# Kernel optimization log

Hardware: AMD Instinct MI355X
Metric: run time of the kernel (lower is better)

The kernel has to match this reference:

```python
import jax, jax.numpy as jnp
import numpy as np

B, C, N = 4, 256, 4096
BN_EPS = 1e-5


def setup_inputs() -> dict:
    key = jax.random.key(0)
    ks = jax.random.split(key, 8)
    Cq = C // 4
    return {
        "x": jax.random.normal(ks[0], (B, C, N), dtype=jnp.float32),
        # q_conv and k_conv share weights (self.q_conv.weight = self.k_conv.weight)
        "w_qk": jax.random.normal(ks[1], (Cq, C), dtype=jnp.float32) * 0.05,
        "w_v": jax.random.normal(ks[2], (C, C), dtype=jnp.float32) * 0.05,
        "b_v": jax.random.normal(ks[3], (C,), dtype=jnp.float32) * 0.05,
        # LBR: Conv1d(C,C,1) + BN1d (inference stats) + ReLU
        "w_lbr": jax.random.normal(ks[4], (C, C), dtype=jnp.float32) * 0.05,
        "b_lbr": jax.random.normal(ks[5], (C,), dtype=jnp.float32) * 0.05,
        "bn_gamma": jnp.ones((C,), dtype=jnp.float32),
        "bn_beta": jnp.zeros((C,), dtype=jnp.float32),
        "bn_mean": jax.random.normal(ks[6], (C,), dtype=jnp.float32) * 0.05,
        "bn_var": jax.random.uniform(ks[7], (C,), dtype=jnp.float32, minval=0.5, maxval=1.5),
    }


def reference(x, w_qk, w_v, b_v, w_lbr, b_lbr, bn_gamma, bn_beta, bn_mean, bn_var):
    # x: [B, C, N]
    chans = x.shape[1]
    # conv1x1 Q/K (shared weight, no bias), V (with bias)
    x_q = jnp.einsum('qc,bcn->bnq', w_qk, x)          # [B, N, C/4]
    x_k = jnp.einsum('qc,bcm->bqm', w_qk, x)          # [B, C/4, N]
    x_v = jnp.einsum('oc,bcn->bon', w_v, x) + b_v[None, :, None]  # [B, C, N]
    # energy: [B, N_query, N_key]
    energy = jnp.einsum('bnq,bqm->bnm', x_q, x_k)
    # 'SL' normalization: scale by C**-0.5, softmax over dim=-2 (query axis)
    energy = energy * (chans ** -0.5)
    attention = jax.nn.softmax(energy, axis=-2)        # [B, N, N]
    # x_r[b,c,m] = sum_n x_v[b,c,n] * attention[b,n,m]
    x_r = jnp.einsum('bcn,bnm->bcm', x_v, attention)   # [B, C, N]
    # offset residual
    x_r = x - x_r
    # LBR: conv1x1 -> BN (inference) -> ReLU
    h = jnp.einsum('oc,bcn->bon', w_lbr, x_r) + b_lbr[None, :, None]
    inv_std = jax.lax.rsqrt(bn_var + BN_EPS)
    h = (h - bn_mean[None, :, None]) * (inv_std * bn_gamma)[None, :, None] + bn_beta[None, :, None]
    h = jax.nn.relu(h)
    return x + h
```

## Files before the change

kernel.cpp:

```cpp
#include <hip/hip_runtime.h>
#include <hip/hip_bf16.h>
#include <stdint.h>
#include <math.h>

#define Bq 4
#define Cc 256
#define Nn 4096
#define CQ 64
#define QKSCALE 0.30028060219661246f
#define NT 64
#define NIT (Nn / NT)
#define QBUF 8704

typedef short s16x4 __attribute__((ext_vector_type(4)));
typedef short s16x8 __attribute__((ext_vector_type(8)));
typedef unsigned int u32x4 __attribute__((ext_vector_type(4)));
typedef float f32x16 __attribute__((ext_vector_type(16)));

#define MFMA32(a,b,c) __builtin_amdgcn_mfma_f32_32x32x16_bf16((a),(b),(c),0,0,0)

#define BAR_LGKM() asm volatile("s_waitcnt lgkmcnt(0)\n\ts_barrier" ::: "memory")

static __device__ __forceinline__ unsigned short f2b(float f) {
  unsigned int u = __float_as_uint(f);
  u += 0x7FFFu + ((u >> 16) & 1u);
  return (unsigned short)(u >> 16);
}

static __device__ __forceinline__ unsigned short f2bh(float f) {
  __hip_bfloat16 h = __float2bfloat16(f);
  return __builtin_bit_cast(unsigned short, h);
}

static __device__ __forceinline__ float b2f(unsigned short u) {
  return __uint_as_float(((unsigned int)u) << 16);
}

static __device__ __forceinline__ float fexp2(float x) {
#if __has_builtin(__builtin_amdgcn_exp2f)
  return __builtin_amdgcn_exp2f(x);
#else
  return exp2f(x);
#endif
}

static __device__ __forceinline__ f32x16 fz16() {
  f32x16 z;
#pragma unroll
  for (int i = 0; i < 16; i++) z[i] = 0.0f;
  return z;
}

__global__ __launch_bounds__(256) void k_prep(
    const float* __restrict__ wqk, const float* __restrict__ wv,
    const float* __restrict__ wlbr, const float* __restrict__ blbr,
    const float* __restrict__ gamma, const float* __restrict__ beta,
    const float* __restrict__ mean, const float* __restrict__ var,
    unsigned short* __restrict__ Wcat, float* __restrict__ sd,
    unsigned int* __restrict__ mxb) {
  int bx = blockIdx.x, t = threadIdx.x;
  if (bx < 576) {
    float v;
    if (bx < 64) v = wqk[bx * 256 + t] * QKSCALE;
    else if (bx < 320) v = wv[(bx - 64) * 256 + t];
    else v = wlbr[(bx - 320) * 256 + t];
    Wcat[bx * 256 + t] = f2b(v);
  } else {
    float s = gamma[t] * rsqrtf(var[t] + 1e-5f);
    sd[t] = s;
    sd[256 + t] = beta[t] + (blbr[t] - mean[t]) * s;
    if (t < 4) mxb[t] = 0u;
  }
}

__global__ __launch_bounds__(640) void k_proj(const float* __restrict__ x,
                                              const unsigned short* __restrict__ Wcat,
                                              const float* __restrict__ bv,
                                              unsigned short* __restrict__ qkT,
                                              unsigned short* __restrict__ Vf,
                                              unsigned short* __restrict__ xT) {
  __shared__ unsigned short xs[32 * 264];
  int bx = blockIdx.x;
  int b = bx >> 7;
  int ntile = bx & 127;
  int n0 = ntile * 32;
  int t = threadIdx.x;
  const float* xb = x + (size_t)b * Cc * Nn;
  for (int u = t; u < 1024; u += 640) {
    int c = u >> 2, j = (u & 3) * 8;
    const float* src = &xb[(size_t)c * Nn + n0 + j];
    float4 v0 = *(const float4*)src;
    float4 v1 = *(const float4*)(src + 4);
    xs[(j + 0) * 264 + c] = f2b(v0.x);
    xs[(j + 1) * 264 + c] = f2b(v0.y);
    xs[(j + 2) * 264 + c] = f2b(v0.z);
    xs[(j + 3) * 264 + c] = f2b(v0.w);
    xs[(j + 4) * 264 + c] = f2b(v1.x);
    xs[(j + 5) * 264 + c] = f2b(v1.y);
    xs[(j + 6) * 264 + c] = f2b(v1.z);
    xs[(j + 7) * 264 + c] = f2b(v1.w);
  }
  int w = t >> 6, a = t & 31, g = (t >> 5) & 1;
  bool isqk = (w >= 8);
  int row0 = isqk ? (w - 8) * 32 : 64 + w * 32;
  s16x8 wf[16];
#pragma unroll
  for (int kc = 0; kc < 16; kc++)
    wf[kc] = *(const s16x8*)&Wcat[(size_t)(row0 + a) * 256 + kc * 16 + 8 * g];
  __syncthreads();
  unsigned short* xTb = xT + ((size_t)b * Nn + n0) * Cc;
  for (int u = t; u < 1024; u += 640) {
    int row = u >> 5, ch = u & 31;
    *(s16x8*)&xTb[(size_t)row * Cc + ch * 8] = *(const s16x8*)&xs[row * 264 + ch * 8];
  }
  f32x16 acc = fz16();
#pragma unroll
  for (int kc = 0; kc < 16; kc++) {
    s16x8 xf = *(const s16x8*)&xs[a * 264 + kc * 16 + 8 * g];
    acc = MFMA32(xf, wf[kc], acc);
  }
  if (isqk) {
    unsigned short* dst = qkT + ((size_t)b * Nn + n0) * CQ;
    int q0 = row0;
#pragma unroll
    for (int r = 0; r < 16; r++) {
      int n = (r & 3) + 8 * (r >> 2) + 4 * g;
      dst[(size_t)n * CQ + q0 + a] = f2b(acc[r]);
    }
  } else {
    int c0 = row0 - 64;
    float bvv = bv[c0 + a];
    s16x8 vlo, vhi;
#pragma unroll
    for (int r = 0; r < 8; r++) {
      vlo[r] = (short)f2b(acc[r] + bvv);
      vhi[r] = (short)f2b(acc[8 + r] + bvv);
    }
    unsigned short* dstF =
        Vf + ((size_t)(b * 128 + ntile) * 4 + g) * 2048 + (size_t)(c0 + a) * 8;
    *(s16x8*)dstF = vlo;
    *(s16x8*)(dstF + 4096) = vhi;
  }
}

__global__ __launch_bounds__(256) void k_norm(const unsigned short* __restrict__ qkT,
                                              float* __restrict__ nrm,
                                              unsigned int* __restrict__ mxb) {
  int idx = blockIdx.x * 256 + threadIdx.x;
  const unsigned short* row = qkT + (size_t)idx * CQ;
  float s = 0.0f;
#pragma unroll
  for (int k = 0; k < 8; k++) {
    s16x8 v = *(const s16x8*)&row[k * 8];
#pragma unroll
    for (int j = 0; j < 8; j++) {
      float f = b2f((unsigned short)v[j]);
      s += f * f;
    }
  }
  float nr = sqrtf(s);
  nrm[idx] = nr;
  float m = nr;
#pragma unroll
  for (int off = 1; off < 64; off <<= 1) m = fmaxf(m, __shfl_xor(m, off, 64));
  __shared__ float wm[4];
  if ((threadIdx.x & 63) == 0) wm[threadIdx.x >> 6] = m;
  __syncthreads();
  if (threadIdx.x == 0) {
    float mm = fmaxf(fmaxf(wm[0], wm[1]), fmaxf(wm[2], wm[3]));
    atomicMax(mxb + (idx >> 12), __float_as_uint(mm));
  }
}

__global__ __launch_bounds__(512, 2) void k_attn(const unsigned short* __restrict__ qkT,
                                                 const unsigned short* __restrict__ Vf,
                                                 const float* __restrict__ nrm,
                                                 const unsigned int* __restrict__ mxb,
                                                 unsigned short* __restrict__ xT) {
  __shared__ __align__(16) char smem[33280];
  int bx = blockIdx.x;
  int id = ((bx & 7) << 6) | (bx >> 3);
  int b = id >> 7;
  int m0 = (id & 127) * 32;
  int t = threadIdx.x;
  int w = t >> 6, a = t & 31, g = (t >> 5) & 1;
  int nh = w >> 2, cs = w & 3;
  bool isProd = (w == 0) | (w == 7);
  unsigned int* Plds = (unsigned int*)(smem + 2 * QBUF);
  const unsigned short* qkTb = qkT + (size_t)b * Nn * CQ;
  int mcol = m0 + a;
  s16x8 Bqk[4];
#pragma unroll
  for (int kc = 0; kc < 4; kc++)
    Bqk[kc] = *(const s16x8*)&qkTb[(size_t)mcol * CQ + kc * 16 + 8 * g];
  float Mh = nrm[(size_t)b * Nn + mcol] * __uint_as_float(mxb[b]) + 0.01f;
  int ccol = cs * 64 + a;
  const unsigned short* Vfb = Vf + (size_t)b * 1048576 + (size_t)g * 2048;

  int qc = t & 7, qr = t >> 3;
  s16x8 qf;
#define STAGE_LOAD(nn)                                                         \
  do {                                                                         \
    qf = *(const s16x8*)&qkTb[(size_t)((nn) + qr) * CQ + qc * 8];              \
  } while (0)
#define STAGE_WRITE(bc)                                                        \
  do {                                                                         \
    unsigned short* Q_ = (unsigned short*)(smem + (bc) * QBUF);                \
    unsigned short* dq = &Q_[qr * 68 + qc * 8];                                \
    *(s16x4*)dq = __builtin_shufflevector(qf, qf, 0, 1, 2, 3);                 \
    *(s16x4*)(dq + 4) = __builtin_shufflevector(qf, qf, 4, 5, 6, 7);           \
  } while (0)

  STAGE_LOAD(0);
  STAGE_WRITE(0);
  STAGE_LOAD(NT);
  f32x16 acc0 = fz16(), acc1 = fz16();
  float Lp = 0.0f;
  BAR_LGKM();
#pragma unroll 1
  for (int ns = 0; ns < NIT; ns++) {
    int cur = ns & 1;
    const unsigned short* Vt = Vfb + (size_t)(ns * 2 + nh) * 8192;
    s16x8 vf0[2], vf1[2];
#pragma unroll
    for (int kk = 0; kk < 2; kk++) {
      vf0[kk] = *(const s16x8*)&Vt[(size_t)kk * 4096 + (size_t)ccol * 8];
      vf1[kk] = *(const s16x8*)&Vt[(size_t)kk * 4096 + (size_t)(ccol + 32) * 8];
    }
    const unsigned short* Qc = (const unsigned short*)(smem + cur * QBUF);
    s16x8 pw0, pw1;
    if (isProd) {
      f32x16 E = fz16();
#pragma unroll
      for (int kc = 0; kc < 4; kc++) {
        const unsigned short* p = &Qc[(nh * 32 + a) * 68 + kc * 16 + 8 * g];
        s16x4 lo = *(const s16x4*)p, hi = *(const s16x4*)(p + 4);
        E = MFMA32(__builtin_shufflevector(lo, hi, 0, 1, 2, 3, 4, 5, 6, 7), Bqk[kc], E);
      }
#pragma unroll
      for (int r = 0; r < 16; r++) E[r] = fexp2(E[r] - Mh);
      Lp += (((E[0] + E[1]) + (E[2] + E[3])) + ((E[4] + E[5]) + (E[6] + E[7]))) +
            (((E[8] + E[9]) + (E[10] + E[11])) + ((E[12] + E[13]) + (E[14] + E[15])));
#pragma unroll
      for (int j = 0; j < 8; j++) {
        pw0[j] = (short)f2bh(E[j]);
        pw1[j] = (short)f2bh(E[8 + j]);
      }
      u32x4 u0 = __builtin_bit_cast(u32x4, pw0);
      u32x4 u1 = __builtin_bit_cast(u32x4, pw1);
      unsigned int* Pq = Plds + nh * 512 + (t & 63);
      Pq[0] = u0[0]; Pq[64] = u0[1]; Pq[128] = u0[2]; Pq[192] = u0[3];
      Pq[256] = u1[0]; Pq[320] = u1[1]; Pq[384] = u1[2]; Pq[448] = u1[3];
    }
    if (ns + 1 < NIT) STAGE_WRITE(cur ^ 1);
    if (ns + 2 < NIT) STAGE_LOAD((ns + 2) * NT);
    BAR_LGKM();
    if (!isProd) {
      const unsigned int* Pq = Plds + nh * 512 + (t & 63);
      u32x4 u0, u1;
      u0[0] = Pq[0]; u0[1] = Pq[64]; u0[2] = Pq[128]; u0[3] = Pq[192];
      u1[0] = Pq[256]; u1[1] = Pq[320]; u1[2] = Pq[384]; u1[3] = Pq[448];
      pw0 = __builtin_bit_cast(s16x8, u0);
      pw1 = __builtin_bit_cast(s16x8, u1);
    }
#pragma unroll
    for (int kk = 0; kk < 2; kk++) {
      s16x8 pk = (kk == 0) ? pw0 : pw1;
      acc0 = MFMA32(pk, vf0[kk], acc0);
      acc1 = MFMA32(pk, vf1[kk], acc1);
    }
    BAR_LGKM();
  }
#undef STAGE_LOAD
#undef STAGE_WRITE
  float Lw = Lp + __shfl_xor(Lp, 32, 64);
  float* Pf = (float*)smem;
  float* Ls = (float*)(smem + 32768);
  if (isProd && (t & 63) < 32) Ls[nh * 32 + a] = Lw;
  if (nh == 1) {
    int base0 = cs * 2048;
#pragma unroll
    for (int r = 0; r < 16; r++) {
      int row = (r & 3) + 8 * (r >> 2) + 4 * g;
      Pf[base0 + row * 64 + a] = acc0[r];
      Pf[base0 + row * 64 + 32 + a] = acc1[r];
    }
  }
  __syncthreads();
  if (nh == 0) {
    unsigned short* xTb = xT + ((size_t)b * Nn + m0) * Cc;
    int base0 = cs * 2048;
#pragma unroll
    for (int r = 0; r < 16; r++) {
      int row = (r & 3) + 8 * (r >> 2) + 4 * g;
      float a0 = acc0[r] + Pf[base0 + row * 64 + a];
      float a1 = acc1[r] + Pf[base0 + row * 64 + 32 + a];
      float rL = 1.0f / (Ls[row] + Ls[32 + row]);
      unsigned short* p0 = &xTb[(size_t)row * Cc + cs * 64 + a];
      unsigned short* p1 = p0 + 32;
      *p0 = f2b(b2f(*p0) - a0 * rL);
      *p1 = f2b(b2f(*p1) - a1 * rL);
    }
  }
}

__global__ __launch_bounds__(512) void k_lbr(const unsigned short* __restrict__ xrT,
                                             const unsigned short* __restrict__ Wcat,
                                             const float* __restrict__ sd,
                                             const float* __restrict__ x,
                                             float* __restrict__ out) {
  __shared__ unsigned short xs[32 * 264];
  __shared__ float sL[256], dL[256];
  int bx = blockIdx.x;
  int b = bx >> 7;
  int n0 = (bx & 127) * 32;
  int t = threadIdx.x;
  const unsigned short* src = xrT + ((size_t)b * Nn + n0) * Cc;
  for (int u = t; u < 1024; u += 512) {
    int row = u >> 5, ch = u & 31;
    *(s16x8*)&xs[row * 264 + ch * 8] = *(const s16x8*)&src[row * Cc + ch * 8];
  }
  if (t < 256) {
    sL[t] = sd[t];
    dL[t] = sd[256 + t];
  }
  int w = t >> 6, a = t & 31, g = (t >> 5) & 1;
  int o0 = w * 32;
  s16x8 wf[16];
#pragma unroll
  for (int kc = 0; kc < 16; kc++)
    wf[kc] = *(const s16x8*)&Wcat[(size_t)(320 + o0 + a) * 256 + kc * 16 + 8 * g];
  __syncthreads();
  f32x16 acc = fz16();
#pragma unroll
  for (int kc = 0; kc < 16; kc++) {
    s16x8 xf = *(const s16x8*)&xs[a * 264 + kc * 16 + 8 * g];
    acc = MFMA32(wf[kc], xf, acc);
  }
  const float* xb = x + (size_t)b * Cc * Nn;
  float* ob = out + (size_t)b * Cc * Nn;
#pragma unroll
  for (int r = 0; r < 16; r++) {
    int o = o0 + (r & 3) + 8 * (r >> 2) + 4 * g;
    float v = acc[r] * sL[o] + dL[o];
    v = fmaxf(v, 0.0f);
    ob[(size_t)o * Nn + n0 + a] = xb[(size_t)o * Nn + n0 + a] + v;
  }
}

extern "C" void kernel_launch(void* const* d_in, const int* in_sizes, int n_in,
                              void* d_out, int out_size, void* d_ws, size_t ws_size,
                              hipStream_t stream) {
  (void)in_sizes; (void)n_in; (void)out_size; (void)ws_size;
  const float* x = (const float*)d_in[0];
  const float* wqk = (const float*)d_in[1];
  const float* wv = (const float*)d_in[2];
  const float* bv = (const float*)d_in[3];
  const float* wlbr = (const float*)d_in[4];
  const float* blbr = (const float*)d_in[5];
  const float* gamma = (const float*)d_in[6];
  const float* beta = (const float*)d_in[7];
  const float* mean = (const float*)d_in[8];
  const float* var = (const float*)d_in[9];
  char* ws = (char*)d_ws;
  unsigned short* qkT = (unsigned short*)ws;
  unsigned short* Vf = (unsigned short*)(ws + 2097152);
  unsigned short* xT = (unsigned short*)(ws + 10485760);
  float* sd = (float*)(ws + 18874368);
  unsigned short* Wcat = (unsigned short*)(ws + 18876416);
  float* out = (float*)d_out;
  float* nrm = (float*)d_out;
  unsigned int* mxb = (unsigned int*)((char*)d_out + 131072);

  k_prep<<<dim3(577), dim3(256), 0, stream>>>(wqk, wv, wlbr, blbr, gamma, beta,
                                              mean, var, Wcat, sd, mxb);
  k_proj<<<dim3(512), dim3(640), 0, stream>>>(x, Wcat, bv, qkT, Vf, xT);
  k_norm<<<dim3(64), dim3(256), 0, stream>>>(qkT, nrm, mxb);
  k_attn<<<dim3(512), dim3(512), 0, stream>>>(qkT, Vf, nrm, mxb, xT );
  k_lbr<<<dim3(512), dim3(512), 0, stream>>>(xT , Wcat, sd, x, out);
}
```

Before: 108.6 us.

## Restructure attention kernel: 64-column tiles, split-N waves, barrier-free main loop

```diff
diff --git a/kernel.cpp b/kernel.cpp
--- a/kernel.cpp
+++ b/kernel.cpp
@@ -8,9 +8,6 @@
 #define Nn 4096
 #define CQ 64
 #define QKSCALE 0.30028060219661246f
-#define NT 64
-#define NIT (Nn / NT)
-#define QBUF 8704
 
 typedef short s16x4 __attribute__((ext_vector_type(4)));
 typedef short s16x8 __attribute__((ext_vector_type(8)));
@@ -18,8 +15,6 @@
 typedef float f32x16 __attribute__((ext_vector_type(16)));
 
 #define MFMA32(a,b,c) __builtin_amdgcn_mfma_f32_32x32x16_bf16((a),(b),(c),0,0,0)
-
-#define BAR_LGKM() asm volatile("s_waitcnt lgkmcnt(0)\n\ts_barrier" ::: "memory")
 
 static __device__ __forceinline__ unsigned short f2b(float f) {
   unsigned int u = __float_as_uint(f);
@@ -49,6 +44,11 @@
 #pragma unroll
   for (int i = 0; i < 16; i++) z[i] = 0.0f;
   return z;
+}
+
+static __device__ __forceinline__ float sum16(f32x16 E) {
+  return (((E[0] + E[1]) + (E[2] + E[3])) + ((E[4] + E[5]) + (E[6] + E[7]))) +
+         (((E[8] + E[9]) + (E[10] + E[11])) + ((E[12] + E[13]) + (E[14] + E[15])));
 }
 
 __global__ __launch_bounds__(256) void k_prep(
@@ -177,130 +177,129 @@
                                                  const float* __restrict__ nrm,
                                                  const unsigned int* __restrict__ mxb,
                                                  unsigned short* __restrict__ xT) {
-  __shared__ __align__(16) char smem[33280];
+  __shared__ __align__(16) float Pf[4 * 128 * 33];
+  __shared__ float Ls[4 * 64];
   int bx = blockIdx.x;
-  int id = ((bx & 7) << 6) | (bx >> 3);
-  int b = id >> 7;
-  int m0 = (id & 127) * 32;
+  int id = ((bx & 7) << 5) | (bx >> 3);
+  int b = id >> 6;
+  int m0 = (id & 63) * 64;
   int t = threadIdx.x;
   int w = t >> 6, a = t & 31, g = (t >> 5) & 1;
-  int nh = w >> 2, cs = w & 3;
-  bool isProd = (w == 0) | (w == 7);
-  unsigned int* Plds = (unsigned int*)(smem + 2 * QBUF);
+  int cs = w >> 2, ns = w & 3;
   const unsigned short* qkTb = qkT + (size_t)b * Nn * CQ;
-  int mcol = m0 + a;
-  s16x8 Bqk[4];
+  s16x8 Bq0[4], Bq1[4];
+#pragma unroll
+  for (int kc = 0; kc < 4; kc++) {
+    Bq0[kc] = *(const s16x8*)&qkTb[(size_t)(m0 + a) * CQ + kc * 16 + 8 * g];
+    Bq1[kc] = *(const s16x8*)&qkTb[(size_t)(m0 + 32 + a) * CQ + kc * 16 + 8 * g];
+  }
+  float mxf = __uint_as_float(mxb[b]);
+  float Mh0 = nrm[(size_t)b * Nn + m0 + a] * mxf + 0.01f;
+  float Mh1 = nrm[(size_t)b * Nn + m0 + 32 + a] * mxf + 0.01f;
+  const unsigned short* Vc = Vf + (size_t)b * 1048576 + (size_t)g * 2048 +
+                             (size_t)(cs * 128 + a) * 8;
+  f32x16 acc[8];
+#pragma unroll
+  for (int i = 0; i < 8; i++) acc[i] = fz16();
+  float Lp0 = 0.0f, Lp1 = 0.0f;
+  s16x8 qf[4];
 #pragma unroll
   for (int kc = 0; kc < 4; kc++)
-    Bqk[kc] = *(const s16x8*)&qkTb[(size_t)mcol * CQ + kc * 16 + 8 * g];
-  float Mh = nrm[(size_t)b * Nn + mcol] * __uint_as_float(mxb[b]) + 0.01f;
-  int ccol = cs * 64 + a;
-  const unsigned short* Vfb = Vf + (size_t)b * 1048576 + (size_t)g * 2048;
-
-  int qc = t & 7, qr = t >> 3;
-  s16x8 qf;
-#define STAGE_LOAD(nn)                                                         \
-  do {                                                                         \
-    qf = *(const s16x8*)&qkTb[(size_t)((nn) + qr) * CQ + qc * 8];              \
-  } while (0)
-#define STAGE_WRITE(bc)                                                        \
-  do {                                                                         \
-    unsigned short* Q_ = (unsigned short*)(smem + (bc) * QBUF);                \
-    unsigned short* dq = &Q_[qr * 68 + qc * 8];                                \
-    *(s16x4*)dq = __builtin_shufflevector(qf, qf, 0, 1, 2, 3);                 \
-    *(s16x4*)(dq + 4) = __builtin_shufflevector(qf, qf, 4, 5, 6, 7);           \
-  } while (0)
-
-  STAGE_LOAD(0);
-  STAGE_WRITE(0);
-  STAGE_LOAD(NT);
-  f32x16 acc0 = fz16(), acc1 = fz16();
-  float Lp = 0.0f;
-  BAR_LGKM();
+    qf[kc] = *(const s16x8*)&qkTb[(size_t)(ns * 32 + a) * CQ + kc * 16 + 8 * g];
 #pragma unroll 1
-  for (int ns = 0; ns < NIT; ns++) {
-    int cur = ns & 1;
-    const unsigned short* Vt = Vfb + (size_t)(ns * 2 + nh) * 8192;
-    s16x8 vf0[2], vf1[2];
-#pragma unroll
-    for (int kk = 0; kk < 2; kk++) {
-      vf0[kk] = *(const s16x8*)&Vt[(size_t)kk * 4096 + (size_t)ccol * 8];
-      vf1[kk] = *(const s16x8*)&Vt[(size_t)kk * 4096 + (size_t)(ccol + 32) * 8];
-    }
-    const unsigned short* Qc = (const unsigned short*)(smem + cur * QBUF);
-    s16x8 pw0, pw1;
-    if (isProd) {
-      f32x16 E = fz16();
-#pragma unroll
-      for (int kc = 0; kc < 4; kc++) {
-        const unsigned short* p = &Qc[(nh * 32 + a) * 68 + kc * 16 + 8 * g];
-        s16x4 lo = *(const s16x4*)p, hi = *(const s16x4*)(p + 4);
-        E = MFMA32(__builtin_shufflevector(lo, hi, 0, 1, 2, 3, 4, 5, 6, 7), Bqk[kc], E);
+  for (int nt = ns; nt < 128; nt += 4) {
+    const unsigned short* Vt = Vc + (size_t)nt * 8192;
+    f32x16 E0 = fz16(), E1 = fz16();
+#pragma unroll
+    for (int kc = 0; kc < 4; kc++) E0 = MFMA32(qf[kc], Bq0[kc], E0);
+    s16x8 va0, va1, va2, va3;
+    va0 = *(const s16x8*)&Vt[0];
+    va1 = *(const s16x8*)&Vt[4096];
+    va2 = *(const s16x8*)&Vt[256];
+    va3 = *(const s16x8*)&Vt[4096 + 256];
+#pragma unroll
+    for (int kc = 0; kc < 4; kc++) E1 = MFMA32(qf[kc], Bq1[kc], E1);
+    int ntn = (nt + 4) & 127;
+#pragma unroll
+    for (int kc = 0; kc < 4; kc++)
+      qf[kc] = *(const s16x8*)&qkTb[(size_t)(ntn * 32 + a) * CQ + kc * 16 + 8 * g];
+#pragma unroll
+    for (int r = 0; r < 16; r++) E0[r] = fexp2(E0[r] - Mh0);
+    Lp0 += sum16(E0);
+    s16x8 p00, p01;
+#pragma unroll
+    for (int j = 0; j < 8; j++) {
+      p00[j] = (short)f2bh(E0[j]);
+      p01[j] = (short)f2bh(E0[8 + j]);
+    }
+#pragma unroll
+    for (int r = 0; r < 16; r++) E1[r] = fexp2(E1[r] - Mh1);
+    Lp1 += sum16(E1);
+    s16x8 p10, p11;
+#pragma unroll
+    for (int j = 0; j < 8; j++) {
+      p10[j] = (short)f2bh(E1[j]);
+      p11[j] = (short)f2bh(E1[8 + j]);
+    }
+    acc[0] = MFMA32(p00, va0, acc[0]);
+    acc[4] = MFMA32(p10, va0, acc[4]);
+    acc[1] = MFMA32(p00, va2, acc[1]);
+    acc[5] = MFMA32(p10, va2, acc[5]);
+    acc[0] = MFMA32(p01, va1, acc[0]);
+    acc[4] = MFMA32(p11, va1, acc[4]);
+    acc[1] = MFMA32(p01, va3, acc[1]);
+    acc[5] = MFMA32(p11, va3, acc[5]);
+    s16x8 vb0, vb1, vb2, vb3;
+    vb0 = *(const s16x8*)&Vt[512];
+    vb1 = *(const s16x8*)&Vt[4096 + 512];
+    vb2 = *(const s16x8*)&Vt[768];
+    vb3 = *(const s16x8*)&Vt[4096 + 768];
+    acc[2] = MFMA32(p00, vb0, acc[2]);
+    acc[6] = MFMA32(p10, vb0, acc[6]);
+    acc[3] = MFMA32(p00, vb2, acc[3]);
+    acc[7] = MFMA32(p10, vb2, acc[7]);
+    acc[2] = MFMA32(p01, vb1, acc[2]);
+    acc[6] = MFMA32(p11, vb1, acc[6]);
+    acc[3] = MFMA32(p01, vb3, acc[3]);
+    acc[7] = MFMA32(p11, vb3, acc[7]);
+  }
+  float Lw0 = Lp0 + __shfl_xor(Lp0, 32, 64);
+  float Lw1 = Lp1 + __shfl_xor(Lp1, 32, 64);
+  if (cs == 0 && (t & 63) < 32) {
+    Ls[ns * 64 + a] = Lw0;
+    Ls[ns * 64 + 32 + a] = Lw1;
+  }
+  unsigned short* xTb = xT + ((size_t)b * Nn + m0) * Cc;
+#pragma unroll
+  for (int q = 0; q < 4; q++) {
+    int qmt = q >> 1, qcs = q & 1;
+    __syncthreads();
+    if (cs == qcs) {
+#pragma unroll
+      for (int ct = 0; ct < 4; ct++) {
+        float* dst = &Pf[(size_t)(ns * 128 + ct * 32 + a) * 33];
+        f32x16 A = acc[qmt * 4 + ct];
+#pragma unroll
+        for (int r = 0; r < 16; r++) {
+          int mrow = (r & 3) + 8 * (r >> 2) + 4 * g;
+          dst[mrow] = A[r];
+        }
       }
-#pragma unroll
-      for (int r = 0; r < 16; r++) E[r] = fexp2(E[r] - Mh);
-      Lp += (((E[0] + E[1]) + (E[2] + E[3])) + ((E[4] + E[5]) + (E[6] + E[7]))) +
-            (((E[8] + E[9]) + (E[10] + E[11])) + ((E[12] + E[13]) + (E[14] + E[15])));
-#pragma unroll
-      for (int j = 0; j < 8; j++) {
-        pw0[j] = (short)f2bh(E[j]);
-        pw1[j] = (short)f2bh(E[8 + j]);
-      }
-      u32x4 u0 = __builtin_bit_cast(u32x4, pw0);
-      u32x4 u1 = __builtin_bit_cast(u32x4, pw1);
-      unsigned int* Pq = Plds + nh * 512 + (t & 63);
-      Pq[0] = u0[0]; Pq[64] = u0[1]; Pq[128] = u0[2]; Pq[192] = u0[3];
-      Pq[256] = u1[0]; Pq[320] = u1[1]; Pq[384] = u1[2]; Pq[448] = u1[3];
-    }
-    if (ns + 1 < NIT) STAGE_WRITE(cur ^ 1);
-    if (ns + 2 < NIT) STAGE_LOAD((ns + 2) * NT);
-    BAR_LGKM();
-    if (!isProd) {
-      const unsigned int* Pq = Plds + nh * 512 + (t & 63);
-      u32x4 u0, u1;
-      u0[0] = Pq[0]; u0[1] = Pq[64]; u0[2] = Pq[128]; u0[3] = Pq[192];
-      u1[0] = Pq[256]; u1[1] = Pq[320]; u1[2] = Pq[384]; u1[3] = Pq[448];
-      pw0 = __builtin_bit_cast(s16x8, u0);
-      pw1 = __builtin_bit_cast(s16x8, u1);
-    }
-#pragma unroll
-    for (int kk = 0; kk < 2; kk++) {
-      s16x8 pk = (kk == 0) ? pw0 : pw1;
-      acc0 = MFMA32(pk, vf0[kk], acc0);
-      acc1 = MFMA32(pk, vf1[kk], acc1);
-    }
-    BAR_LGKM();
-  }
-#undef STAGE_LOAD
-#undef STAGE_WRITE
-  float Lw = Lp + __shfl_xor(Lp, 32, 64);
-  float* Pf = (float*)smem;
-  float* Ls = (float*)(smem + 32768);
-  if (isProd && (t & 63) < 32) Ls[nh * 32 + a] = Lw;
-  if (nh == 1) {
-    int base0 = cs * 2048;
-#pragma unroll
-    for (int r = 0; r < 16; r++) {
-      int row = (r & 3) + 8 * (r >> 2) + 4 * g;
-      Pf[base0 + row * 64 + a] = acc0[r];
-      Pf[base0 + row * 64 + 32 + a] = acc1[r];
-    }
-  }
-  __syncthreads();
-  if (nh == 0) {
-    unsigned short* xTb = xT + ((size_t)b * Nn + m0) * Cc;
-    int base0 = cs * 2048;
-#pragma unroll
-    for (int r = 0; r < 16; r++) {
-      int row = (r & 3) + 8 * (r >> 2) + 4 * g;
-      float a0 = acc0[r] + Pf[base0 + row * 64 + a];
-      float a1 = acc1[r] + Pf[base0 + row * 64 + 32 + a];
-      float rL = 1.0f / (Ls[row] + Ls[32 + row]);
-      unsigned short* p0 = &xTb[(size_t)row * Cc + cs * 64 + a];
-      unsigned short* p1 = p0 + 32;
-      *p0 = f2b(b2f(*p0) - a0 * rL);
-      *p1 = f2b(b2f(*p1) - a1 * rL);
-    }
+    }
+    __syncthreads();
+    int m = t & 31, c8 = t >> 5;
+    float rL = 1.0f / (((Ls[qmt * 32 + m] + Ls[64 + qmt * 32 + m]) +
+                        (Ls[128 + qmt * 32 + m] + Ls[192 + qmt * 32 + m])));
+    unsigned short* xrow = &xTb[(size_t)(qmt * 32 + m) * Cc + qcs * 128 + c8 * 8];
+    s16x8 xv = *(const s16x8*)xrow;
+#pragma unroll
+    for (int j = 0; j < 8; j++) {
+      int cl = c8 * 8 + j;
+      float s = ((Pf[(0 * 128 + cl) * 33 + m] + Pf[(1 * 128 + cl) * 33 + m]) +
+                 (Pf[(2 * 128 + cl) * 33 + m] + Pf[(3 * 128 + cl) * 33 + m]));
+      xv[j] = (short)f2b(b2f((unsigned short)xv[j]) - s * rL);
+    }
+    *(s16x8*)xrow = xv;
   }
 }
 
@@ -376,6 +375,6 @@
                                               mean, var, Wcat, sd, mxb);
   k_proj<<<dim3(512), dim3(640), 0, stream>>>(x, Wcat, bv, qkT, Vf, xT);
   k_norm<<<dim3(64), dim3(256), 0, stream>>>(qkT, nrm, mxb);
-  k_attn<<<dim3(512), dim3(512), 0, stream>>>(qkT, Vf, nrm, mxb, xT );
+  k_attn<<<dim3(256), dim3(512), 0, stream>>>(qkT, Vf, nrm, mxb, xT );
   k_lbr<<<dim3(512), dim3(512), 0, stream>>>(xT , Wcat, sd, x, out);
 }
```

Measured after the change: 101.0 us. -7.0%, faster.
